# Kernel optimization log

Hardware: AMD Instinct MI355X
Metric: run time of the kernel (lower is better)

Reference implementation:

```python
import jax, jax.numpy as jnp
import numpy as np

N_HEAD = 16
N_EMBD = 1024
B, T = 4, 2048


def setup_inputs() -> dict:
    key = jax.random.key(0)
    ks = jax.random.split(key, 5)
    s_in = 1.0 / np.sqrt(N_EMBD)
    return {
        "x": jax.random.normal(ks[0], (B, T, N_EMBD), dtype=jnp.float32),
        "W_qkv": jax.random.normal(ks[1], (N_EMBD, 3 * N_EMBD), dtype=jnp.float32) * s_in,
        "b_qkv": jnp.zeros((3 * N_EMBD,), dtype=jnp.float32),
        "W_proj": jax.random.normal(ks[2], (N_EMBD, N_EMBD), dtype=jnp.float32) * s_in,
        "b_proj": jnp.zeros((N_EMBD,), dtype=jnp.float32),
    }


def reference(x, W_qkv, b_qkv, W_proj, b_proj):
    Bb, Tt, C = x.shape
    H = N_HEAD
    hd = C // H  # head dim
    qkv = x @ W_qkv + b_qkv                      # [B,T,3C]
    q, k, v = jnp.split(qkv, 3, axis=-1)
    # [B,H,T,hd]
    q = q.reshape(Bb, Tt, H, hd).transpose(0, 2, 1, 3)
    k = k.reshape(Bb, Tt, H, hd).transpose(0, 2, 1, 3)
    v = v.reshape(Bb, Tt, H, hd).transpose(0, 2, 1, 3)
    scale = 1.0 / np.sqrt(hd).astype(np.float32)
    att = jnp.einsum("bhqd,bhkd->bhqk", q, k) * scale
    causal = jnp.tril(jnp.ones((Tt, Tt), dtype=bool))
    att = jnp.where(causal, att, jnp.float32(-jnp.inf))
    att = jax.nn.softmax(att, axis=-1)
    y = jnp.einsum("bhqk,bhkd->bhqd", att, v)    # [B,H,T,hd]
    y = y.transpose(0, 2, 1, 3).reshape(Bb, Tt, C)
    return y @ W_proj + b_proj
```

## Files before the change

kernel.cpp:

```cpp
#include <hip/hip_runtime.h>
#include <hip/hip_bf16.h>
#include <math.h>

typedef unsigned short u16;
typedef _Float16 f16_t;
typedef f16_t f16x8 __attribute__((ext_vector_type(8)));
typedef float f32x4 __attribute__((ext_vector_type(4)));

#define N_HEADC 16
#define C_EMBD  1024
#define B_SZ    4
#define T_SEQ   2048
#define HD      64
#define M_TOT   (B_SZ * T_SEQ)

#define BM 128
#define BN 256
#define BK 32
#define NT (C_EMBD / BK)
#define A_T (BM * BK)
#define B_T (BN * BK)

#define SWZ_CHUNK(l) ((((l) & 3) ^ (((l) >> 3) & 3)) * 8)

__device__ __forceinline__ u16 f2h(float f) {
    f16_t h = (f16_t)f;
    return __builtin_bit_cast(u16, h);
}
__device__ __forceinline__ unsigned pkf16(float a, float b) {
    unsigned lo = f2h(a), hi = f2h(b);
    return lo | (hi << 16);
}
__device__ __forceinline__ float fexp2(float x) {
#if __has_builtin(__builtin_amdgcn_exp2f)
    return __builtin_amdgcn_exp2f(x);
#else
    return exp2f(x);
#endif
}
__device__ __forceinline__ void gl_lds16(const u16* g, u16* l) {
    __builtin_amdgcn_global_load_lds(
        (const __attribute__((address_space(1))) unsigned int*)g,
        (__attribute__((address_space(3))) unsigned int*)l,
        16, 0, 0);
}

__global__ __launch_bounds__(256) void prep(const float* __restrict__ x,
                                            const float* __restrict__ Wqkv,
                                            const float* __restrict__ Wproj,
                                            u16* __restrict__ xh,
                                            u16* __restrict__ WqkvT,
                                            u16* __restrict__ WprojT) {
    __shared__ float tile[32][33];
    int bid = blockIdx.x, tid = threadIdx.x;
    if (bid < 8192) {
        int i = bid * 1024 + tid * 4;
        float4 v = *(const float4*)(x + i);
        ushort4 o;
        o.x = f2h(v.x); o.y = f2h(v.y); o.z = f2h(v.z); o.w = f2h(v.w);
        *(ushort4*)(xh + i) = o;
        return;
    }
    const float* in; u16* outp; int N, bx, by;
    if (bid < 8192 + 3072) {
        int b2 = bid - 8192; bx = b2 % 96; by = b2 / 96;
        in = Wqkv; outp = WqkvT; N = 3 * C_EMBD;
    } else {
        int b2 = bid - 11264; bx = b2 % 32; by = b2 / 32;
        in = Wproj; outp = WprojT; N = C_EMBD;
    }
    int tx = tid & 31, ty = tid >> 5;
    int n0 = bx * 32, k0 = by * 32;
    for (int i = ty; i < 32; i += 8)
        tile[i][tx] = in[(size_t)(k0 + i) * N + n0 + tx];
    __syncthreads();
    for (int i = ty; i < 32; i += 8)
        outp[(size_t)(n0 + i) * C_EMBD + k0 + tx] = f2h(tile[tx][i]);
}

#define GEMM_PROLOGUE(Ap, BTp)                                                  \
    int m0 = blockIdx.y * BM;                                                   \
    int n0 = blockIdx.x * BN;                                                   \
    int tid = threadIdx.x;                                                      \
    int w = tid >> 6, lane = tid & 63;                                          \
    int wm = w >> 2, wn = w & 3;                                                \
    int quad = lane >> 4, rl = lane & 15;                                       \
    int srow = lane >> 2, sko = SWZ_CHUNK(lane);                                \
    int kx = (rl >> 1) & 3;                       \
    int qx = (quad ^ kx) * 8;                                                   \
    f32x4 acc[4][4];                                                            \
    _Pragma("unroll")                                                           \
    for (int i = 0; i < 4; ++i)                                                 \
        _Pragma("unroll")                                                       \
        for (int j = 0; j < 4; ++j)                                             \
            acc[i][j] = f32x4{0.f, 0.f, 0.f, 0.f};                              \
    const u16* gA  = Ap  + (size_t)(m0 + w * 16 + srow) * C_EMBD + sko;         \
    const u16* gB0 = BTp + (size_t)(n0 + w * 16 + srow) * C_EMBD + sko;         \
    const u16* gB1 = gB0 + (size_t)128 * C_EMBD;                                \
    u16* lA = sA + w * 512;                                                     \
    u16* lB = sB + w * 512;                                                     \
                                        \
    gl_lds16(gA,      lA);                                                      \
    gl_lds16(gB0,     lB);                                                      \
    gl_lds16(gB1,     lB + 128 * BK);                                           \
    gl_lds16(gA + BK,  lA + A_T);                                               \
    gl_lds16(gB0 + BK, lB + B_T);                                               \
    gl_lds16(gB1 + BK, lB + B_T + 128 * BK);                                    \
    gA += 2 * BK; gB0 += 2 * BK; gB1 += 2 * BK;                                 \
    int bufR = 0, bufS = 2;                                                     \
    for (int t = 0; t < NT; ++t) {                                              \
        if (t == NT - 1) asm volatile("s_waitcnt vmcnt(0)" ::: "memory");       \
        else             asm volatile("s_waitcnt vmcnt(3)" ::: "memory");       \
        asm volatile("s_barrier" ::: "memory");                                 \
        const u16* pA = sA + bufR * A_T + (wm * 64) * BK;                       \
        const u16* pB = sB + bufR * B_T + (wn * 64) * BK;                       \
        f16x8 af[4], bfr[4];                                                    \
        _Pragma("unroll")                                                       \
        for (int i = 0; i < 4; ++i)                                             \
            af[i] = *(const f16x8*)&pA[(i * 16 + rl) * BK + qx];                \
        _Pragma("unroll")                                                       \
        for (int j = 0; j < 4; ++j)                                             \
            bfr[j] = *(const f16x8*)&pB[(j * 16 + rl) * BK + qx];               \
        if (t + 2 < NT) {                                                       \
            u16* dA = sA + bufS * A_T + w * 512;                                \
            u16* dB = sB + bufS * B_T + w * 512;                                \
            gl_lds16(gA,  dA);                                                  \
            gl_lds16(gB0, dB);                                                  \
            gl_lds16(gB1, dB + 128 * BK);                                       \
            gA += BK; gB0 += BK; gB1 += BK;                                     \
        }                                                                       \
        __builtin_amdgcn_s_setprio(1);                                          \
        _Pragma("unroll")                                                       \
        for (int i = 0; i < 4; ++i)                                             \
            _Pragma("unroll")                                                   \
            for (int j = 0; j < 4; ++j)                                         \
                acc[i][j] = __builtin_amdgcn_mfma_f32_16x16x32_f16(             \
                    af[i], bfr[j], acc[i][j], 0, 0, 0);                         \
        __builtin_amdgcn_s_setprio(0);                                          \
        bufR = bufR == 2 ? 0 : bufR + 1;                                        \
        bufS = bufS == 2 ? 0 : bufS + 1;                                        \
    }

__global__ __launch_bounds__(512) void gemm_qkv(const u16* __restrict__ A,
                                                const u16* __restrict__ BT,
                                                const float* __restrict__ bias,
                                                u16* __restrict__ qQ,
                                                u16* __restrict__ qK,
                                                u16* __restrict__ qVt) {
    __shared__ __align__(16) u16 sA[3 * A_T];
    __shared__ __align__(16) u16 sB[3 * B_T];
    GEMM_PROLOGUE(A, BT)

    const float QSC = 0.18033688011112042f;
    int p = n0 >> 10;
    if (p < 2) {
        u16* dst = p == 0 ? qQ : qK;
        float sc = p == 0 ? QSC : 1.0f;
        #pragma unroll
        for (int j = 0; j < 4; ++j) {
            int n = n0 + wn * 64 + j * 16 + rl;
            float bv = bias[n];
            int cch = n & 1023;
            int h = cch >> 6, d = cch & 63;
            #pragma unroll
            for (int i = 0; i < 4; ++i) {
                int mbase = m0 + wm * 64 + i * 16 + quad * 4;
                int bb = mbase >> 11, t0 = mbase & 2047;
                size_t thbase = ((size_t)bb * N_HEADC + h) * T_SEQ;
                #pragma unroll
                for (int r = 0; r < 4; ++r)
                    dst[(thbase + t0 + r) * HD + d] = f2h((acc[i][j][r] + bv) * sc);
            }
        }
    } else {
        u16 (*tr)[136] = (u16 (*)[136])sA;
        int bb = m0 >> 11, t0g = m0 & 2047;
        #pragma unroll
        for (int c = 0; c < 4; ++c) {
            __syncthreads();
            if (wn == c) {
                #pragma unroll
                for (int j = 0; j < 4; ++j) {
                    int rowr = j * 16 + rl;
                    float bv = bias[n0 + c * 64 + rowr];
                    #pragma unroll
                    for (int i = 0; i < 4; ++i) {
                        int mm = wm * 64 + i * 16 + quad * 4;
                        *(unsigned*)&tr[rowr][mm]     = pkf16(acc[i][j][0] + bv, acc[i][j][1] + bv);
                        *(unsigned*)&tr[rowr][mm + 2] = pkf16(acc[i][j][2] + bv, acc[i][j][3] + bv);
                    }
                }
            }
            __syncthreads();
            #pragma unroll
            for (int s = 0; s < 2; ++s) {
                int task = s * 512 + tid;
                int nn = task >> 4, seg = task & 15;
                int ch = (n0 & 1023) + c * 64 + nn;
                int h = ch >> 6, d = ch & 63;
                size_t di = (((size_t)bb * N_HEADC + h) * HD + d) * T_SEQ + t0g + seg * 8;
                *(uint4*)&qVt[di] = *(const uint4*)&tr[nn][seg * 8];
            }
        }
    }
}

__global__ __launch_bounds__(512) void gemm_proj(const u16* __restrict__ A,
                                                 const u16* __restrict__ BT,
                                                 const float* __restrict__ bias,
                                                 float* __restrict__ out) {
    __shared__ __align__(16) u16 sA[3 * A_T];
    __shared__ __align__(16) u16 sB[3 * B_T];
    GEMM_PROLOGUE(A, BT)

    #pragma unroll
    for (int i = 0; i < 4; ++i) {
        int mbase = m0 + wm * 64 + i * 16 + quad * 4;
        #pragma unroll
        for (int j = 0; j < 4; ++j) {
            int n = n0 + wn * 64 + j * 16 + rl;
            float bv = bias[n];
            #pragma unroll
            for (int r = 0; r < 4; ++r)
                out[(size_t)(mbase + r) * C_EMBD + n] = acc[i][j][r] + bv;
        }
    }
}

__global__ __launch_bounds__(256) void attn_mfma(const u16* __restrict__ Qg,
                                                 const u16* __restrict__ Kg,
                                                 const u16* __restrict__ Vtg,
                                                 u16* __restrict__ yh) {
    int bid = blockIdx.x;
    int bx = bid >> 6;
    int g  = bid & 63;
    int h = g & 15, b = g >> 4;
    const size_t hs = (size_t)T_SEQ * HD;
    const u16* Qp  = Qg  + ((size_t)b * N_HEADC + h) * hs;
    const u16* Kp  = Kg  + ((size_t)b * N_HEADC + h) * hs;
    const u16* Vtp = Vtg + ((size_t)b * N_HEADC + h) * hs;

    __shared__ __align__(16) u16 sK[2][2][64][32];
    __shared__ __align__(16) u16 sVt[2][2][64][32];
    __shared__ __align__(16) u16 sP[4][32][72];

    int tid = threadIdx.x;
    int lane = tid & 63, w = tid >> 6;
    int quad = lane >> 4, rl = lane & 15;
    int kx = (rl >> 1) & 3;
    int qx = (quad ^ kx) * 8;
    u16* sPw = &sP[w][0][0];
    int srow = lane >> 2;
    int sch = SWZ_CHUNK(lane);
    const f32x4 mneg = {-4.f, -4.f, -4.f, -4.f};

    const u16* gp0[4];
    u16* ld0[4]; u16* ld1[4];
    int gstep;
    if (w < 2) {
        gstep = 64 * HD;
        #pragma unroll
        for (int c = 0; c < 4; ++c) {
            gp0[c] = Kp + (size_t)(c * 16 + srow) * HD + w * 32 + sch;
            ld0[c] = &sK[0][w][c * 16][0];
            ld1[c] = &sK[1][w][c * 16][0];
        }
    } else {
        gstep = 64;
        #pragma unroll
        for (int c = 0; c < 4; ++c) {
            gp0[c] = Vtp + (size_t)(c * 16 + srow) * T_SEQ + (w - 2) * 32 + sch;
            ld0[c] = &sVt[0][w - 2][c * 16][0];
            ld1[c] = &sVt[1][w - 2][c * 16][0];
        }
    }

    #pragma unroll
    for (int phase = 0; phase < 2; ++phase) {
        int qt = phase == 0 ? (15 - bx) : bx;
        int q0w = qt * 128 + w * 32;
        int nkt = 2 * qt + 2;

        f16x8 qf[2][2];
        #pragma unroll
        for (int nt = 0; nt < 2; ++nt)
            #pragma unroll
            for (int ks = 0; ks < 2; ++ks)
                qf[nt][ks] = *(const f16x8*)&Qp[(size_t)(q0w + nt * 16 + rl) * HD + ks * 32 + quad * 8];

        f32x4 O[2][4];
        #pragma unroll
        for (int mi = 0; mi < 2; ++mi)
            #pragma unroll
            for (int nd = 0; nd < 4; ++nd)
                O[mi][nd] = f32x4{0.f, 0.f, 0.f, 0.f};
        float l_[2] = {0.f, 0.f};

        const u16* gp[4];
        #pragma unroll
        for (int c = 0; c < 4; ++c) gp[c] = gp0[c];

        __syncthreads();
        #pragma unroll
        for (int c = 0; c < 4; ++c) gl_lds16(gp[c], ld0[c]);

        for (int kt = 0; kt < nkt; ++kt) {
            __syncthreads();
            int buf = kt & 1;
            int k0 = kt * 64;
            if (kt + 1 < nkt) {
                u16* const* ldn = ((kt + 1) & 1) ? ld1 : ld0;
                #pragma unroll
                for (int c = 0; c < 4; ++c) {
                    gp[c] += gstep;
                    gl_lds16(gp[c], ldn[c]);
                }
            }
            if (k0 > q0w + 31) continue;

            f32x4 st[4][2];
            #pragma unroll
            for (int mt = 0; mt < 4; ++mt) {
                f16x8 ak0 = *(const f16x8*)&sK[buf][0][mt * 16 + rl][qx];
                f16x8 ak1 = *(const f16x8*)&sK[buf][1][mt * 16 + rl][qx];
                #pragma unroll
                for (int nt = 0; nt < 2; ++nt) {
                    f32x4 t = __builtin_amdgcn_mfma_f32_16x16x32_f16(ak0, qf[nt][0], mneg, 0, 0, 0);
                    st[mt][nt] = __builtin_amdgcn_mfma_f32_16x16x32_f16(ak1, qf[nt][1], t, 0, 0, 0);
                }
            }

            if (k0 + 63 > q0w) {
                #pragma unroll
                for (int mt = 0; mt < 4; ++mt)
                    #pragma unroll
                    for (int nt = 0; nt < 2; ++nt)
                        #pragma unroll
                        for (int r = 0; r < 4; ++r) {
                            int kpos = k0 + mt * 16 + quad * 4 + r;
                            int q = q0w + nt * 16 + rl;
                            if (kpos > q) st[mt][nt][r] = -INFINITY;
                        }
            }

            #pragma unroll
            for (int nt = 0; nt < 2; ++nt) {
                float lsum = 0.f;
                #pragma unroll
                for (int mt = 0; mt < 4; ++mt) {
                    float p0 = fexp2(st[mt][nt][0]);
                    float p1 = fexp2(st[mt][nt][1]);
                    float p2 = fexp2(st[mt][nt][2]);
                    float p3 = fexp2(st[mt][nt][3]);
                    lsum += (p0 + p1) + (p2 + p3);
                    *(uint2*)&sPw[(nt * 16 + rl) * 72 + mt * 16 + quad * 4] =
                        make_uint2(pkf16(p0, p1), pkf16(p2, p3));
                }
                l_[nt] += lsum;
            }

            #pragma unroll
            for (int ks = 0; ks < 2; ++ks) {
                f16x8 ap0 = *(const f16x8*)&sPw[(0 * 16 + rl) * 72 + ks * 32 + quad * 8];
                f16x8 ap1 = *(const f16x8*)&sPw[(1 * 16 + rl) * 72 + ks * 32 + quad * 8];
                #pragma unroll
                for (int nd = 0; nd < 4; ++nd) {
                    f16x8 bv = *(const f16x8*)&sVt[buf][ks][nd * 16 + rl][qx];
                    O[0][nd] = __builtin_amdgcn_mfma_f32_16x16x32_f16(ap0, bv, O[0][nd], 0, 0, 0);
                    O[1][nd] = __builtin_amdgcn_mfma_f32_16x16x32_f16(ap1, bv, O[1][nd], 0, 0, 0);
                }
            }
        }

        #pragma unroll
        for (int nt = 0; nt < 2; ++nt) {
            l_[nt] += __shfl_xor(l_[nt], 16);
            l_[nt] += __shfl_xor(l_[nt], 32);
        }
        float linv[2] = {1.f / l_[0], 1.f / l_[1]};
        int idxq = quad * 4;
        #pragma unroll
        for (int mi = 0; mi < 2; ++mi)
            #pragma unroll
            for (int r = 0; r < 4; ++r) {
                float li = __shfl(linv[mi], idxq + r);
                int qg = q0w + mi * 16 + quad * 4 + r;
                size_t base = ((size_t)b * T_SEQ + qg) * C_EMBD + h * HD;
                #pragma unroll
                for (int nd = 0; nd < 4; ++nd)
                    yh[base + nd * 16 + rl] = f2h(O[mi][nd][r] * li);
            }
    }
}

extern "C" void kernel_launch(void* const* d_in, const int* in_sizes, int n_in,
                              void* d_out, int out_size, void* d_ws, size_t ws_size,
                              hipStream_t stream) {
    const float* x     = (const float*)d_in[0];
    const float* Wqkv  = (const float*)d_in[1];
    const float* bqkv  = (const float*)d_in[2];
    const float* Wproj = (const float*)d_in[3];
    const float* bproj = (const float*)d_in[4];
    float* out = (float*)d_out;

    char* ws = (char*)d_ws;
    u16* xh     = (u16*)(ws);
    u16* WqkvT  = (u16*)(ws + (size_t)16 * 1024 * 1024);
    u16* WprojT = (u16*)(ws + (size_t)22 * 1024 * 1024);
    u16* qQ     = (u16*)(ws + (size_t)24 * 1024 * 1024);
    u16* qK     = (u16*)(ws + (size_t)40 * 1024 * 1024);
    u16* qVt    = (u16*)(ws + (size_t)56 * 1024 * 1024);
    u16* yh     = (u16*)(ws + (size_t)72 * 1024 * 1024);

    prep<<<dim3(12288), dim3(256), 0, stream>>>(x, Wqkv, Wproj, xh, WqkvT, WprojT);
    gemm_qkv<<<dim3(3 * C_EMBD / BN, M_TOT / BM), dim3(512), 0, stream>>>(
        xh, WqkvT, bqkv, qQ, qK, qVt);
    attn_mfma<<<dim3(512), dim3(256), 0, stream>>>(
        qQ, qK, qVt, yh);
    gemm_proj<<<dim3(C_EMBD / BN, M_TOT / BM), dim3(512), 0, stream>>>(
        yh, WprojT, bproj, out);
}
```

Before: 260.9 us.

## Process paired causal query tiles concurrently in 8-wave attention blocks sharing K/V

The attention kernel used to process its two complementary query tiles (15-j and j) one after the other, streaming K/V twice. Now each block has 8 waves: four handle the long tile and four handle the short tile at the same time. Both groups share one double-buffered K/V stream, so the K/V tiles are loaded once per block and each wave issues half as many global-to-LDS copies. Block indices are also remapped so the pair assignments are interleaved. The cost is that the short-tile waves sit idle at barriers once they pass their causal limit, and the larger blocks need more registers and LDS, which may lower occupancy.

```diff
diff --git a/kernel.cpp b/kernel.cpp
--- a/kernel.cpp
+++ b/kernel.cpp
@@ -227,13 +227,14 @@
     }
 }
 
-__global__ __launch_bounds__(256) void attn_mfma(const u16* __restrict__ Qg,
+__global__ __launch_bounds__(512) void attn_mfma(const u16* __restrict__ Qg,
                                                  const u16* __restrict__ Kg,
                                                  const u16* __restrict__ Vtg,
                                                  u16* __restrict__ yh) {
     int bid = blockIdx.x;
-    int bx = bid >> 6;
+    int a  = bid >> 6;
     int g  = bid & 63;
+    int j  = a < 4 ? a : 11 - a;
     int h = g & 15, b = g >> 4;
     const size_t hs = (size_t)T_SEQ * HD;
     const u16* Qp  = Qg  + ((size_t)b * N_HEADC + h) * hs;
@@ -242,7 +243,7 @@
 
     __shared__ __align__(16) u16 sK[2][2][64][32];
     __shared__ __align__(16) u16 sVt[2][2][64][32];
-    __shared__ __align__(16) u16 sP[4][32][72];
+    __shared__ __align__(16) u16 sP[8][32][72];
 
     int tid = threadIdx.x;
     int lane = tid & 63, w = tid >> 6;
@@ -254,143 +255,140 @@
     int sch = SWZ_CHUNK(lane);
     const f32x4 mneg = {-4.f, -4.f, -4.f, -4.f};
 
-    const u16* gp0[4];
-    u16* ld0[4]; u16* ld1[4];
+    int qt  = (w < 4) ? (15 - j) : j;
+    int q0w = qt * 128 + (w & 3) * 32;
+    int nkt = 2 * (15 - j) + 2;
+
+    const u16* gp[2];
+    u16* ld0[2]; u16* ld1[2];
     int gstep;
-    if (w < 2) {
+    if (w < 4) {
         gstep = 64 * HD;
-        #pragma unroll
-        for (int c = 0; c < 4; ++c) {
-            gp0[c] = Kp + (size_t)(c * 16 + srow) * HD + w * 32 + sch;
-            ld0[c] = &sK[0][w][c * 16][0];
-            ld1[c] = &sK[1][w][c * 16][0];
+        int half = (w >> 1) & 1, rbase = (w & 1) * 32;
+        #pragma unroll
+        for (int c = 0; c < 2; ++c) {
+            int r = rbase + c * 16;
+            gp[c]  = Kp + (size_t)(r + srow) * HD + half * 32 + sch;
+            ld0[c] = &sK[0][half][r][0];
+            ld1[c] = &sK[1][half][r][0];
         }
     } else {
         gstep = 64;
-        #pragma unroll
-        for (int c = 0; c < 4; ++c) {
-            gp0[c] = Vtp + (size_t)(c * 16 + srow) * T_SEQ + (w - 2) * 32 + sch;
-            ld0[c] = &sVt[0][w - 2][c * 16][0];
-            ld1[c] = &sVt[1][w - 2][c * 16][0];
-        }
-    }
-
+        int v = w - 4;
+        int half = (v >> 1) & 1, rbase = (v & 1) * 32;
+        #pragma unroll
+        for (int c = 0; c < 2; ++c) {
+            int r = rbase + c * 16;
+            gp[c]  = Vtp + (size_t)(r + srow) * T_SEQ + half * 32 + sch;
+            ld0[c] = &sVt[0][half][r][0];
+            ld1[c] = &sVt[1][half][r][0];
+        }
+    }
+
+    f16x8 qf[2][2];
     #pragma unroll
-    for (int phase = 0; phase < 2; ++phase) {
-        int qt = phase == 0 ? (15 - bx) : bx;
-        int q0w = qt * 128 + w * 32;
-        int nkt = 2 * qt + 2;
-
-        f16x8 qf[2][2];
-        #pragma unroll
-        for (int nt = 0; nt < 2; ++nt)
-            #pragma unroll
-            for (int ks = 0; ks < 2; ++ks)
-                qf[nt][ks] = *(const f16x8*)&Qp[(size_t)(q0w + nt * 16 + rl) * HD + ks * 32 + quad * 8];
-
-        f32x4 O[2][4];
-        #pragma unroll
-        for (int mi = 0; mi < 2; ++mi)
+    for (int nt = 0; nt < 2; ++nt)
+        #pragma unroll
+        for (int ks = 0; ks < 2; ++ks)
+            qf[nt][ks] = *(const f16x8*)&Qp[(size_t)(q0w + nt * 16 + rl) * HD + ks * 32 + quad * 8];
+
+    f32x4 O[2][4];
+    #pragma unroll
+    for (int mi = 0; mi < 2; ++mi)
+        #pragma unroll
+        for (int nd = 0; nd < 4; ++nd)
+            O[mi][nd] = f32x4{0.f, 0.f, 0.f, 0.f};
+    float l_[2] = {0.f, 0.f};
+
+    gl_lds16(gp[0], ld0[0]);
+    gl_lds16(gp[1], ld0[1]);
+
+    for (int kt = 0; kt < nkt; ++kt) {
+        __syncthreads();
+        int buf = kt & 1;
+        int k0 = kt * 64;
+        if (kt + 1 < nkt) {
+            u16* const* ldn = ((kt + 1) & 1) ? ld1 : ld0;
+            #pragma unroll
+            for (int c = 0; c < 2; ++c) {
+                gp[c] += gstep;
+                gl_lds16(gp[c], ldn[c]);
+            }
+        }
+        if (k0 > q0w + 31) continue;
+
+        f32x4 st[4][2];
+        #pragma unroll
+        for (int mt = 0; mt < 4; ++mt) {
+            f16x8 ak0 = *(const f16x8*)&sK[buf][0][mt * 16 + rl][qx];
+            f16x8 ak1 = *(const f16x8*)&sK[buf][1][mt * 16 + rl][qx];
+            #pragma unroll
+            for (int nt = 0; nt < 2; ++nt) {
+                f32x4 t = __builtin_amdgcn_mfma_f32_16x16x32_f16(ak0, qf[nt][0], mneg, 0, 0, 0);
+                st[mt][nt] = __builtin_amdgcn_mfma_f32_16x16x32_f16(ak1, qf[nt][1], t, 0, 0, 0);
+            }
+        }
+
+        if (k0 + 63 > q0w) {
+            #pragma unroll
+            for (int mt = 0; mt < 4; ++mt)
+                #pragma unroll
+                for (int nt = 0; nt < 2; ++nt)
+                    #pragma unroll
+                    for (int r = 0; r < 4; ++r) {
+                        int kpos = k0 + mt * 16 + quad * 4 + r;
+                        int q = q0w + nt * 16 + rl;
+                        if (kpos > q) st[mt][nt][r] = -INFINITY;
+                    }
+        }
+
+        #pragma unroll
+        for (int nt = 0; nt < 2; ++nt) {
+            float lsum = 0.f;
+            #pragma unroll
+            for (int mt = 0; mt < 4; ++mt) {
+                float p0 = fexp2(st[mt][nt][0]);
+                float p1 = fexp2(st[mt][nt][1]);
+                float p2 = fexp2(st[mt][nt][2]);
+                float p3 = fexp2(st[mt][nt][3]);
+                lsum += (p0 + p1) + (p2 + p3);
+                *(uint2*)&sPw[(nt * 16 + rl) * 72 + mt * 16 + quad * 4] =
+                    make_uint2(pkf16(p0, p1), pkf16(p2, p3));
+            }
+            l_[nt] += lsum;
+        }
+
+        #pragma unroll
+        for (int ks = 0; ks < 2; ++ks) {
+            f16x8 ap0 = *(const f16x8*)&sPw[(0 * 16 + rl) * 72 + ks * 32 + quad * 8];
+            f16x8 ap1 = *(const f16x8*)&sPw[(1 * 16 + rl) * 72 + ks * 32 + quad * 8];
+            #pragma unroll
+            for (int nd = 0; nd < 4; ++nd) {
+                f16x8 bv = *(const f16x8*)&sVt[buf][ks][nd * 16 + rl][qx];
+                O[0][nd] = __builtin_amdgcn_mfma_f32_16x16x32_f16(ap0, bv, O[0][nd], 0, 0, 0);
+                O[1][nd] = __builtin_amdgcn_mfma_f32_16x16x32_f16(ap1, bv, O[1][nd], 0, 0, 0);
+            }
+        }
+    }
+
+    #pragma unroll
+    for (int nt = 0; nt < 2; ++nt) {
+        l_[nt] += __shfl_xor(l_[nt], 16);
+        l_[nt] += __shfl_xor(l_[nt], 32);
+    }
+    float linv[2] = {1.f / l_[0], 1.f / l_[1]};
+    int idxq = quad * 4;
+    #pragma unroll
+    for (int mi = 0; mi < 2; ++mi)
+        #pragma unroll
+        for (int r = 0; r < 4; ++r) {
+            float li = __shfl(linv[mi], idxq + r);
+            int qg = q0w + mi * 16 + quad * 4 + r;
+            size_t base = ((size_t)b * T_SEQ + qg) * C_EMBD + h * HD;
             #pragma unroll
             for (int nd = 0; nd < 4; ++nd)
-                O[mi][nd] = f32x4{0.f, 0.f, 0.f, 0.f};
-        float l_[2] = {0.f, 0.f};
-
-        const u16* gp[4];
-        #pragma unroll
-        for (int c = 0; c < 4; ++c) gp[c] = gp0[c];
-
-        __syncthreads();
-        #pragma unroll
-        for (int c = 0; c < 4; ++c) gl_lds16(gp[c], ld0[c]);
-
-        for (int kt = 0; kt < nkt; ++kt) {
-            __syncthreads();
-            int buf = kt & 1;
-            int k0 = kt * 64;
-            if (kt + 1 < nkt) {
-                u16* const* ldn = ((kt + 1) & 1) ? ld1 : ld0;
-                #pragma unroll
-                for (int c = 0; c < 4; ++c) {
-                    gp[c] += gstep;
-                    gl_lds16(gp[c], ldn[c]);
-                }
-            }
-            if (k0 > q0w + 31) continue;
-
-            f32x4 st[4][2];
-            #pragma unroll
-            for (int mt = 0; mt < 4; ++mt) {
-                f16x8 ak0 = *(const f16x8*)&sK[buf][0][mt * 16 + rl][qx];
-                f16x8 ak1 = *(const f16x8*)&sK[buf][1][mt * 16 + rl][qx];
-                #pragma unroll
-                for (int nt = 0; nt < 2; ++nt) {
-                    f32x4 t = __builtin_amdgcn_mfma_f32_16x16x32_f16(ak0, qf[nt][0], mneg, 0, 0, 0);
-                    st[mt][nt] = __builtin_amdgcn_mfma_f32_16x16x32_f16(ak1, qf[nt][1], t, 0, 0, 0);
-                }
-            }
-
-            if (k0 + 63 > q0w) {
-                #pragma unroll
-                for (int mt = 0; mt < 4; ++mt)
-                    #pragma unroll
-                    for (int nt = 0; nt < 2; ++nt)
-                        #pragma unroll
-                        for (int r = 0; r < 4; ++r) {
-                            int kpos = k0 + mt * 16 + quad * 4 + r;
-                            int q = q0w + nt * 16 + rl;
-                            if (kpos > q) st[mt][nt][r] = -INFINITY;
-                        }
-            }
-
-            #pragma unroll
-            for (int nt = 0; nt < 2; ++nt) {
-                float lsum = 0.f;
-                #pragma unroll
-                for (int mt = 0; mt < 4; ++mt) {
-                    float p0 = fexp2(st[mt][nt][0]);
-                    float p1 = fexp2(st[mt][nt][1]);
-                    float p2 = fexp2(st[mt][nt][2]);
-                    float p3 = fexp2(st[mt][nt][3]);
-                    lsum += (p0 + p1) + (p2 + p3);
-                    *(uint2*)&sPw[(nt * 16 + rl) * 72 + mt * 16 + quad * 4] =
-                        make_uint2(pkf16(p0, p1), pkf16(p2, p3));
-                }
-                l_[nt] += lsum;
-            }
-
-            #pragma unroll
-            for (int ks = 0; ks < 2; ++ks) {
-                f16x8 ap0 = *(const f16x8*)&sPw[(0 * 16 + rl) * 72 + ks * 32 + quad * 8];
-                f16x8 ap1 = *(const f16x8*)&sPw[(1 * 16 + rl) * 72 + ks * 32 + quad * 8];
-                #pragma unroll
-                for (int nd = 0; nd < 4; ++nd) {
-                    f16x8 bv = *(const f16x8*)&sVt[buf][ks][nd * 16 + rl][qx];
-                    O[0][nd] = __builtin_amdgcn_mfma_f32_16x16x32_f16(ap0, bv, O[0][nd], 0, 0, 0);
-                    O[1][nd] = __builtin_amdgcn_mfma_f32_16x16x32_f16(ap1, bv, O[1][nd], 0, 0, 0);
-                }
-            }
-        }
-
-        #pragma unroll
-        for (int nt = 0; nt < 2; ++nt) {
-            l_[nt] += __shfl_xor(l_[nt], 16);
-            l_[nt] += __shfl_xor(l_[nt], 32);
-        }
-        float linv[2] = {1.f / l_[0], 1.f / l_[1]};
-        int idxq = quad * 4;
-        #pragma unroll
-        for (int mi = 0; mi < 2; ++mi)
-            #pragma unroll
-            for (int r = 0; r < 4; ++r) {
-                float li = __shfl(linv[mi], idxq + r);
-                int qg = q0w + mi * 16 + quad * 4 + r;
-                size_t base = ((size_t)b * T_SEQ + qg) * C_EMBD + h * HD;
-                #pragma unroll
-                for (int nd = 0; nd < 4; ++nd)
-                    yh[base + nd * 16 + rl] = f2h(O[mi][nd][r] * li);
-            }
-    }
+                yh[base + nd * 16 + rl] = f2h(O[mi][nd][r] * li);
+        }
 }
 
 extern "C" void kernel_launch(void* const* d_in, const int* in_sizes, int n_in,
@@ -415,7 +413,7 @@
     prep<<<dim3(12288), dim3(256), 0, stream>>>(x, Wqkv, Wproj, xh, WqkvT, WprojT);
     gemm_qkv<<<dim3(3 * C_EMBD / BN, M_TOT / BM), dim3(512), 0, stream>>>(
         xh, WqkvT, bqkv, qQ, qK, qVt);
-    attn_mfma<<<dim3(512), dim3(256), 0, stream>>>(
+    attn_mfma<<<dim3(512), dim3(512), 0, stream>>>(
         qQ, qK, qVt, yh);
     gemm_proj<<<dim3(C_EMBD / BN, M_TOT / BM), dim3(512), 0, stream>>>(
         yh, WprojT, bproj, out);
```

New measurement: 236.9 us. 9.2% less time.
